# Optimization experiments

Measured on AMD Instinct MI355X. Metric: run time of the kernel, lower is better.

Reference implementation:

```python
import jax, jax.numpy as jnp
import numpy as np

COMMITMENT_COST = 0.25
NUM_EMBEDDINGS = 8192
EMBEDDING_DIM = 256


def setup_inputs() -> dict:
    key = jax.random.key(0)
    kx, ke = jax.random.split(key)
    x = jax.random.normal(kx, (16, 1024, EMBEDDING_DIM), dtype=jnp.float32)
    # nn.Embedding weight initialized uniform(-1/K, 1/K)
    embedding = jax.random.uniform(
        ke, (NUM_EMBEDDINGS, EMBEDDING_DIM), dtype=jnp.float32,
        minval=-1.0 / NUM_EMBEDDINGS, maxval=1.0 / NUM_EMBEDDINGS)
    return {"x": x, "embedding": embedding}


def reference(x, embedding):
    x_shape = x.shape
    D = embedding.shape[1]
    K = embedding.shape[0]
    flat_x = x.reshape(-1, D)                      # [N, D]
    N = flat_x.shape[0]

    distances = (jnp.sum(flat_x ** 2, axis=1, keepdims=True)
                 + jnp.sum(embedding ** 2, axis=1)
                 - 2.0 * jnp.matmul(flat_x, embedding.T))
    encoding_indices = jnp.argmin(distances, axis=1)  # [N]

    # one-hot @ embedding == gather
    quantized = embedding[encoding_indices].reshape(x_shape)

    sg = jax.lax.stop_gradient
    e_latent_loss = jnp.mean((sg(quantized) - x) ** 2)
    q_latent_loss = jnp.mean((quantized - sg(x)) ** 2)
    loss = q_latent_loss + COMMITMENT_COST * e_latent_loss

    # straight-through estimator
    quantized_st = x + sg(quantized - x)

    # perplexity from mean one-hot usage
    counts = jnp.zeros((K,), dtype=jnp.float32).at[encoding_indices].add(1.0)
    avg_probs = counts / N
    perplexity = jnp.exp(-jnp.sum(avg_probs * jnp.log(avg_probs + 1e-10)))

    return quantized_st.reshape(x_shape), loss, perplexity
```

## Files before the change

### kernel.cpp

```cpp
#include <hip/hip_runtime.h>


#define VQ_N 16384
#define VQ_D 256
#define VQ_K 8192

typedef __attribute__((ext_vector_type(4))) int i32x4;

#define SX 22.0f
#define SEF 1040384.0f
#define C2 (-8.73808386e-08f)

__device__ inline int q8(float f, float scale) {
  return __float2int_rn(fminf(fmaxf(f * scale, -127.f), 127.f));
}

__global__ __launch_bounds__(256) void vq_pack(
    const float* __restrict__ E, signed char* __restrict__ Ebs,
    float* __restrict__ enorm, double* __restrict__ loss_sum,
    int* __restrict__ hist, unsigned int* __restrict__ ticket) {
  const int gid = blockIdx.x * 256 + threadIdx.x;
  if (gid < VQ_K) hist[gid] = 0;
  if (gid == 0) { *loss_sum = 0.0; *ticket = 0u; }
  const int code = gid >> 4;
  const int chunk = gid & 15;
  const float* src = E + (size_t)code * VQ_D + chunk * 16;
  double s = 0.0;
  unsigned int w[4];
#pragma unroll
  for (int v = 0; v < 4; ++v) {
    const float4 f = *(const float4*)(src + v * 4);
    s += (double)f.x * f.x + (double)f.y * f.y + (double)f.z * f.z +
         (double)f.w * f.w;
    const int q0 = q8(f.x, SEF), q1 = q8(f.y, SEF);
    const int q2 = q8(f.z, SEF), q3 = q8(f.w, SEF);
    w[v] = (unsigned)(q0 & 255) | ((unsigned)(q1 & 255) << 8) |
           ((unsigned)(q2 & 255) << 16) | ((unsigned)(q3 & 255) << 24);
  }
  const size_t off =
      ((size_t)(code >> 4) * 16 + chunk) * 256 + (size_t)(code & 15) * 16;
  *(uint4*)(Ebs + off) = make_uint4(w[0], w[1], w[2], w[3]);
#pragma unroll
  for (int m = 1; m <= 8; m <<= 1) s += __shfl_xor(s, m, 64);
  if (chunk == 0) enorm[code] = (float)s;
}

__global__ __launch_bounds__(256, 2) void vq_main(
    const float* __restrict__ X, const signed char* __restrict__ Ebs,
    const float* __restrict__ enorm, const float* __restrict__ Ef,
    float* __restrict__ outq, double* __restrict__ loss_sum,
    int* __restrict__ hist, unsigned int* __restrict__ ticket,
    float* __restrict__ out) {
  __shared__ float red_s[4][32];
  __shared__ int red_i[4][32];
  __shared__ int kfin[32];
  __shared__ double wsum[4];
  __shared__ double part[256];
  __shared__ int sdone;

  const int tid = threadIdx.x;
  const int wave = tid >> 6;
  const int lane = tid & 63;
  const int quad = lane >> 4;
  const int c15 = lane & 15;
  const int r0 = blockIdx.x * 32;

  i32x4 af[2][4];
#pragma unroll
  for (int t = 0; t < 2; ++t) {
    const float* xr = X + (size_t)(r0 + t * 16 + c15) * VQ_D + quad * 16;
#pragma unroll
    for (int m = 0; m < 4; ++m) {
      const float* p = xr + m * 64;
      i32x4 pk;
#pragma unroll
      for (int v = 0; v < 4; ++v) {
        const float4 f = *(const float4*)(p + v * 4);
        const int q0 = q8(f.x, SX), q1 = q8(f.y, SX);
        const int q2 = q8(f.z, SX), q3 = q8(f.w, SX);
        pk[v] = (q0 & 255) | ((q1 & 255) << 8) | ((q2 & 255) << 16) |
                ((q3 & 255) << 24);
      }
      af[t][m] = pk;
    }
  }

  float best_s[2][4];
  int best_i[2][4];
#pragma unroll
  for (int t = 0; t < 2; ++t)
#pragma unroll
    for (int r = 0; r < 4; ++r) { best_s[t][r] = 3.4e38f; best_i[t][r] = 0; }

  const signed char* bp =
      Ebs + (size_t)wave * 4096 + (size_t)quad * 256 + (size_t)c15 * 16;
  int code = wave * 16 + c15;

#define LOADB(buf, en, ptr, cd)                                              \
  {                                                                          \
    _Pragma("unroll") for (int m = 0; m < 4; ++m)                            \
        buf[m] = *(const i32x4*)((ptr) + m * 1024);                          \
    en = enorm[(cd)];                                                        \
  }

#define COMPUTE(buf, en, cd)                                                 \
  {                                                                          \
    i32x4 a0 = {0, 0, 0, 0}, a1 = {0, 0, 0, 0};                              \
    _Pragma("unroll") for (int m = 0; m < 4; ++m) {                          \
      a0 = __builtin_amdgcn_mfma_i32_16x16x64_i8(af[0][m], buf[m], a0, 0, 0, 0); \
      a1 = __builtin_amdgcn_mfma_i32_16x16x64_i8(af[1][m], buf[m], a1, 0, 0, 0); \
    }                                                                        \
    _Pragma("unroll") for (int r = 0; r < 4; ++r) {                          \
      float s;                                                               \
      s = fmaf((float)a0[r], C2, en);                                        \
      if (s < best_s[0][r]) { best_s[0][r] = s; best_i[0][r] = (cd); }       \
      s = fmaf((float)a1[r], C2, en);                                        \
      if (s < best_s[1][r]) { best_s[1][r] = s; best_i[1][r] = (cd); }       \
    }                                                                        \
  }

  i32x4 bb0[4], bb1[4];
  float en0, en1;
  LOADB(bb0, en0, bp, code);
#pragma unroll 1
  for (int i = 0; i < 128; i += 2) {
    LOADB(bb1, en1, bp + 16384, code + 64);
    COMPUTE(bb0, en0, code);
    if (i + 2 < 128) LOADB(bb0, en0, bp + 32768, code + 128);
    COMPUTE(bb1, en1, code + 64);
    bp += 32768;
    code += 128;
  }
#undef LOADB
#undef COMPUTE

#pragma unroll
  for (int t = 0; t < 2; ++t)
#pragma unroll
    for (int r = 0; r < 4; ++r) {
      float s = best_s[t][r];
      int i = best_i[t][r];
#pragma unroll
      for (int m = 1; m <= 8; m <<= 1) {
        const float os = __shfl_xor(s, m, 64);
        const int oi = __shfl_xor(i, m, 64);
        if (os < s || (os == s && oi < i)) { s = os; i = oi; }
      }
      if (c15 == 0) {
        red_s[wave][t * 16 + quad * 4 + r] = s;
        red_i[wave][t * 16 + quad * 4 + r] = i;
      }
    }
  __syncthreads();

  if (tid < 32) {
    float bs = red_s[0][tid];
    int bi = red_i[0][tid];
#pragma unroll
    for (int w = 1; w < 4; ++w) {
      const float s = red_s[w][tid];
      const int i = red_i[w][tid];
      if (s < bs || (s == bs && i < bi)) { bs = s; bi = i; }
    }
    kfin[tid] = bi;
    __hip_atomic_fetch_add(&hist[bi], 1, __ATOMIC_RELAXED,
                           __HIP_MEMORY_SCOPE_AGENT);
  }
  __syncthreads();

  double lacc = 0.0;
#pragma unroll
  for (int j = 0; j < 8; ++j) {
    const int rl = wave * 8 + j;
    const int k = kfin[rl];
    const float4 q = *(const float4*)(Ef + (size_t)k * VQ_D + lane * 4);
    const float4 x =
        *(const float4*)(X + (size_t)(r0 + rl) * VQ_D + lane * 4);
    *(float4*)(outq + (size_t)(r0 + rl) * VQ_D + lane * 4) = q;
    const double dx = (double)q.x - x.x, dy = (double)q.y - x.y;
    const double dz = (double)q.z - x.z, dw = (double)q.w - x.w;
    lacc += dx * dx + dy * dy + dz * dz + dw * dw;
  }
#pragma unroll
  for (int off = 32; off > 0; off >>= 1) lacc += __shfl_down(lacc, off, 64);
  if (lane == 0) wsum[wave] = lacc;
  __syncthreads();
  if (tid == 0) {
    atomicAdd(loss_sum, wsum[0] + wsum[1] + wsum[2] + wsum[3]);
    __threadfence();
    const unsigned int old = __hip_atomic_fetch_add(
        ticket, 1u, __ATOMIC_ACQ_REL, __HIP_MEMORY_SCOPE_AGENT);
    sdone = (old == 511u) ? 1 : 0;
  }
  __syncthreads();

  if (sdone) {
    double s = 0.0;
    for (int k = tid; k < VQ_K; k += 256) {
      const int c = __hip_atomic_load(&hist[k], __ATOMIC_RELAXED,
                                      __HIP_MEMORY_SCOPE_AGENT);
      if (c > 0) {
        const double pr = (double)c * (1.0 / (double)VQ_N);
        s += pr * log(pr + 1e-10);
      }
    }
    part[tid] = s;
    __syncthreads();
    for (int off = 128; off > 0; off >>= 1) {
      if (tid < off) part[tid] += part[tid + off];
      __syncthreads();
    }
    if (tid == 0) {
      const double ls = __hip_atomic_load(loss_sum, __ATOMIC_RELAXED,
                                          __HIP_MEMORY_SCOPE_AGENT);
      out[(size_t)VQ_N * VQ_D] =
          (float)(1.25 * ls / ((double)VQ_N * (double)VQ_D));
      out[(size_t)VQ_N * VQ_D + 1] = (float)exp(-part[0]);
    }
  }
}

extern "C" void kernel_launch(void* const* d_in, const int* in_sizes, int n_in,
                              void* d_out, int out_size, void* d_ws,
                              size_t ws_size, hipStream_t stream) {
  const float* X = (const float*)d_in[0];
  const float* E = (const float*)d_in[1];
  float* out = (float*)d_out;

  char* ws = (char*)d_ws;
  signed char* Ebs = (signed char*)ws;
  float* enorm = (float*)(ws + 2097152);
  double* loss_sum = (double*)(ws + 2129920);
  int* hist = (int*)(ws + 2129984);
  unsigned int* ticket = (unsigned int*)(ws + 2162752);

  vq_pack<<<512, 256, 0, stream>>>(E, Ebs, enorm, loss_sum, hist, ticket);
  vq_main<<<512, 256, 0, stream>>>(X, Ebs, enorm, E, out, loss_sum, hist,
                                   ticket, out);
}
```

Before: 170.4 us.

## Double rows per block, integer-domain distance compare, deeper codebook prefetch

Each block now handles 64 rows instead of 32, so every loaded codebook tile feeds four MFMA row-groups. That halves global codebook traffic per row and halves the grid to 256 blocks. The codebook norms are prescaled into integers so the per-candidate score becomes an integer subtract-compare instead of a convert plus fma. The load pipeline holds four codebook buffers in flight rather than two. The costs are more registers (occupancy hint dropped to 1) and only 256 blocks, which may underfill the GPU, plus a small rounding change in the norm term.

```diff
diff --git a/kernel.cpp b/kernel.cpp
--- a/kernel.cpp
+++ b/kernel.cpp
@@ -9,7 +9,7 @@
 
 #define SX 22.0f
 #define SEF 1040384.0f
-#define C2 (-8.73808386e-08f)
+#define ENSCALE 11444224.0
 
 __device__ inline int q8(float f, float scale) {
   return __float2int_rn(fminf(fmaxf(f * scale, -127.f), 127.f));
@@ -17,7 +17,7 @@
 
 __global__ __launch_bounds__(256) void vq_pack(
     const float* __restrict__ E, signed char* __restrict__ Ebs,
-    float* __restrict__ enorm, double* __restrict__ loss_sum,
+    int* __restrict__ en_int, double* __restrict__ loss_sum,
     int* __restrict__ hist, unsigned int* __restrict__ ticket) {
   const int gid = blockIdx.x * 256 + threadIdx.x;
   if (gid < VQ_K) hist[gid] = 0;
@@ -42,18 +42,18 @@
   *(uint4*)(Ebs + off) = make_uint4(w[0], w[1], w[2], w[3]);
 #pragma unroll
   for (int m = 1; m <= 8; m <<= 1) s += __shfl_xor(s, m, 64);
-  if (chunk == 0) enorm[code] = (float)s;
-}
-
-__global__ __launch_bounds__(256, 2) void vq_main(
+  if (chunk == 0) en_int[code] = (int)__double2int_rn(s * ENSCALE);
+}
+
+__global__ __launch_bounds__(256, 1) void vq_main(
     const float* __restrict__ X, const signed char* __restrict__ Ebs,
-    const float* __restrict__ enorm, const float* __restrict__ Ef,
+    const int* __restrict__ en_int, const float* __restrict__ Ef,
     float* __restrict__ outq, double* __restrict__ loss_sum,
     int* __restrict__ hist, unsigned int* __restrict__ ticket,
     float* __restrict__ out) {
-  __shared__ float red_s[4][32];
-  __shared__ int red_i[4][32];
-  __shared__ int kfin[32];
+  __shared__ int red_s[4][64];
+  __shared__ int red_i[4][64];
+  __shared__ int kfin[64];
   __shared__ double wsum[4];
   __shared__ double part[256];
   __shared__ int sdone;
@@ -63,11 +63,11 @@
   const int lane = tid & 63;
   const int quad = lane >> 4;
   const int c15 = lane & 15;
-  const int r0 = blockIdx.x * 32;
-
-  i32x4 af[2][4];
-#pragma unroll
-  for (int t = 0; t < 2; ++t) {
+  const int r0 = blockIdx.x * 64;
+
+  i32x4 af[4][4];
+#pragma unroll
+  for (int t = 0; t < 4; ++t) {
     const float* xr = X + (size_t)(r0 + t * 16 + c15) * VQ_D + quad * 16;
 #pragma unroll
     for (int m = 0; m < 4; ++m) {
@@ -85,64 +85,75 @@
     }
   }
 
-  float best_s[2][4];
-  int best_i[2][4];
-#pragma unroll
-  for (int t = 0; t < 2; ++t)
-#pragma unroll
-    for (int r = 0; r < 4; ++r) { best_s[t][r] = 3.4e38f; best_i[t][r] = 0; }
+  int best_s[4][4];
+  int best_i[4][4];
+#pragma unroll
+  for (int t = 0; t < 4; ++t)
+#pragma unroll
+    for (int r = 0; r < 4; ++r) { best_s[t][r] = 0x7fffffff; best_i[t][r] = 0; }
 
   const signed char* bp =
       Ebs + (size_t)wave * 4096 + (size_t)quad * 256 + (size_t)c15 * 16;
-  int code = wave * 16 + c15;
-
-#define LOADB(buf, en, ptr, cd)                                              \
+  const int* enp = en_int + wave * 16 + c15;
+  int lidx = 0;
+  int ccode = wave * 16 + c15;
+
+#define LOADB(buf, en)                                                       \
   {                                                                          \
+    const signed char* p_ = bp + (size_t)lidx * 16384;                       \
     _Pragma("unroll") for (int m = 0; m < 4; ++m)                            \
-        buf[m] = *(const i32x4*)((ptr) + m * 1024);                          \
-    en = enorm[(cd)];                                                        \
-  }
-
-#define COMPUTE(buf, en, cd)                                                 \
+        buf[m] = *(const i32x4*)(p_ + m * 1024);                             \
+    en = enp[lidx * 64];                                                     \
+    ++lidx;                                                                  \
+  }
+
+#define COMPUTE(buf, en)                                                     \
   {                                                                          \
     i32x4 a0 = {0, 0, 0, 0}, a1 = {0, 0, 0, 0};                              \
+    i32x4 a2 = {0, 0, 0, 0}, a3 = {0, 0, 0, 0};                              \
     _Pragma("unroll") for (int m = 0; m < 4; ++m) {                          \
       a0 = __builtin_amdgcn_mfma_i32_16x16x64_i8(af[0][m], buf[m], a0, 0, 0, 0); \
       a1 = __builtin_amdgcn_mfma_i32_16x16x64_i8(af[1][m], buf[m], a1, 0, 0, 0); \
+      a2 = __builtin_amdgcn_mfma_i32_16x16x64_i8(af[2][m], buf[m], a2, 0, 0, 0); \
+      a3 = __builtin_amdgcn_mfma_i32_16x16x64_i8(af[3][m], buf[m], a3, 0, 0, 0); \
     }                                                                        \
     _Pragma("unroll") for (int r = 0; r < 4; ++r) {                          \
-      float s;                                                               \
-      s = fmaf((float)a0[r], C2, en);                                        \
-      if (s < best_s[0][r]) { best_s[0][r] = s; best_i[0][r] = (cd); }       \
-      s = fmaf((float)a1[r], C2, en);                                        \
-      if (s < best_s[1][r]) { best_s[1][r] = s; best_i[1][r] = (cd); }       \
+      int s;                                                                 \
+      s = en - a0[r];                                                        \
+      if (s < best_s[0][r]) { best_s[0][r] = s; best_i[0][r] = ccode; }      \
+      s = en - a1[r];                                                        \
+      if (s < best_s[1][r]) { best_s[1][r] = s; best_i[1][r] = ccode; }      \
+      s = en - a2[r];                                                        \
+      if (s < best_s[2][r]) { best_s[2][r] = s; best_i[2][r] = ccode; }      \
+      s = en - a3[r];                                                        \
+      if (s < best_s[3][r]) { best_s[3][r] = s; best_i[3][r] = ccode; }      \
     }                                                                        \
-  }
-
-  i32x4 bb0[4], bb1[4];
-  float en0, en1;
-  LOADB(bb0, en0, bp, code);
+    ccode += 64;                                                             \
+  }
+
+  i32x4 bb0[4], bb1[4], bb2[4], bb3[4];
+  int en0, en1, en2, en3;
+  LOADB(bb0, en0); LOADB(bb1, en1); LOADB(bb2, en2); LOADB(bb3, en3);
 #pragma unroll 1
-  for (int i = 0; i < 128; i += 2) {
-    LOADB(bb1, en1, bp + 16384, code + 64);
-    COMPUTE(bb0, en0, code);
-    if (i + 2 < 128) LOADB(bb0, en0, bp + 32768, code + 128);
-    COMPUTE(bb1, en1, code + 64);
-    bp += 32768;
-    code += 128;
-  }
+  for (int i = 0; i < 124; i += 4) {
+    COMPUTE(bb0, en0); LOADB(bb0, en0);
+    COMPUTE(bb1, en1); LOADB(bb1, en1);
+    COMPUTE(bb2, en2); LOADB(bb2, en2);
+    COMPUTE(bb3, en3); LOADB(bb3, en3);
+  }
+  COMPUTE(bb0, en0); COMPUTE(bb1, en1); COMPUTE(bb2, en2); COMPUTE(bb3, en3);
 #undef LOADB
 #undef COMPUTE
 
 #pragma unroll
-  for (int t = 0; t < 2; ++t)
+  for (int t = 0; t < 4; ++t)
 #pragma unroll
     for (int r = 0; r < 4; ++r) {
-      float s = best_s[t][r];
+      int s = best_s[t][r];
       int i = best_i[t][r];
 #pragma unroll
       for (int m = 1; m <= 8; m <<= 1) {
-        const float os = __shfl_xor(s, m, 64);
+        const int os = __shfl_xor(s, m, 64);
         const int oi = __shfl_xor(i, m, 64);
         if (os < s || (os == s && oi < i)) { s = os; i = oi; }
       }
@@ -153,12 +164,12 @@
     }
   __syncthreads();
 
-  if (tid < 32) {
-    float bs = red_s[0][tid];
+  if (tid < 64) {
+    int bs = red_s[0][tid];
     int bi = red_i[0][tid];
 #pragma unroll
     for (int w = 1; w < 4; ++w) {
-      const float s = red_s[w][tid];
+      const int s = red_s[w][tid];
       const int i = red_i[w][tid];
       if (s < bs || (s == bs && i < bi)) { bs = s; bi = i; }
     }
@@ -170,8 +181,8 @@
 
   double lacc = 0.0;
 #pragma unroll
-  for (int j = 0; j < 8; ++j) {
-    const int rl = wave * 8 + j;
+  for (int j = 0; j < 16; ++j) {
+    const int rl = wave * 16 + j;
     const int k = kfin[rl];
     const float4 q = *(const float4*)(Ef + (size_t)k * VQ_D + lane * 4);
     const float4 x =
@@ -190,7 +201,7 @@
     __threadfence();
     const unsigned int old = __hip_atomic_fetch_add(
         ticket, 1u, __ATOMIC_ACQ_REL, __HIP_MEMORY_SCOPE_AGENT);
-    sdone = (old == 511u) ? 1 : 0;
+    sdone = (old == 255u) ? 1 : 0;
   }
   __syncthreads();
 
@@ -229,12 +240,12 @@
 
   char* ws = (char*)d_ws;
   signed char* Ebs = (signed char*)ws;
-  float* enorm = (float*)(ws + 2097152);
+  int* en_int = (int*)(ws + 2097152);
   double* loss_sum = (double*)(ws + 2129920);
   int* hist = (int*)(ws + 2129984);
   unsigned int* ticket = (unsigned int*)(ws + 2162752);
 
-  vq_pack<<<512, 256, 0, stream>>>(E, Ebs, enorm, loss_sum, hist, ticket);
-  vq_main<<<512, 256, 0, stream>>>(X, Ebs, enorm, E, out, loss_sum, hist,
+  vq_pack<<<512, 256, 0, stream>>>(E, Ebs, en_int, loss_sum, hist, ticket);
+  vq_main<<<256, 256, 0, stream>>>(X, Ebs, en_int, E, out, loss_sum, hist,
                                    ticket, out);
 }
```

Result: faster. 159.7 us (-6.2%).
